# Kernel tuning notes

Hardware: AMD Instinct MI355X
Metric: run time of the kernel (lower is better)

The kernel has to match this reference:

```python
import jax, jax.numpy as jnp
import numpy as np

D_MODEL = 768
NUM_HEADS = 12
HEAD_DIM = D_MODEL // NUM_HEADS
B, S = 2, 2048


def setup_inputs() -> dict:
    key = jax.random.key(0)
    ks = jax.random.split(key, 12)
    s = 1.0 / np.sqrt(D_MODEL)
    inp = {
        "query": jax.random.normal(ks[0], (B, S, D_MODEL), jnp.float32),
        "key": jax.random.normal(ks[1], (B, S, D_MODEL), jnp.float32),
        "value": jax.random.normal(ks[2], (B, S, D_MODEL), jnp.float32),
        # causal mask; masked_fill(scores, mask == 0, -inf)
        "mask": jnp.tril(jnp.ones((S, S), jnp.int32))[None, None, :, :],
        "Wq": jax.random.uniform(ks[3], (D_MODEL, D_MODEL), jnp.float32, -s, s),
        "bq": jax.random.uniform(ks[4], (D_MODEL,), jnp.float32, -s, s),
        "Wk": jax.random.uniform(ks[5], (D_MODEL, D_MODEL), jnp.float32, -s, s),
        "bk": jax.random.uniform(ks[6], (D_MODEL,), jnp.float32, -s, s),
        "Wv": jax.random.uniform(ks[7], (D_MODEL, D_MODEL), jnp.float32, -s, s),
        "bv": jax.random.uniform(ks[8], (D_MODEL,), jnp.float32, -s, s),
        "Wo": jax.random.uniform(ks[9], (D_MODEL, D_MODEL), jnp.float32, -s, s),
        "bo": jax.random.uniform(ks[10], (D_MODEL,), jnp.float32, -s, s),
    }
    return inp


def reference(query, key, value, mask, Wq, bq, Wk, bk, Wv, bv, Wo, bo):
    Bq, Lq, Dm = query.shape
    Lk = key.shape[1]
    H, Dh = NUM_HEADS, HEAD_DIM
    # projections (torch Linear: x @ W.T + b), split into heads -> [B,H,L,Dh]
    q = (query @ Wq.T + bq).reshape(Bq, Lq, H, Dh).transpose(0, 2, 1, 3)
    k = (key @ Wk.T + bk).reshape(Bq, Lk, H, Dh).transpose(0, 2, 1, 3)
    v = (value @ Wv.T + bv).reshape(Bq, Lk, H, Dh).transpose(0, 2, 1, 3)
    scores = jnp.einsum("bhqd,bhkd->bhqk", q, k) / jnp.sqrt(jnp.float32(Dh))
    scores = jnp.where(mask == 0, -jnp.inf, scores)
    attn = jax.nn.softmax(scores, axis=-1)
    context = jnp.einsum("bhqk,bhkd->bhqd", attn, v)
    context = context.transpose(0, 2, 1, 3).reshape(Bq, Lq, Dm)
    return context @ Wo.T + bo
```

## Files before the change

### kernel.cpp

```cpp
#include <hip/hip_runtime.h>

#define DM    768
#define NH    12
#define NB    2
#define DHD   64
#define SQL   2048
#define MROWS 4096
#define WSZ   589824
#define XSZ   3145728
#define QSCALE 0.18033688f

typedef short  s16x8 __attribute__((ext_vector_type(8)));
typedef float  f32x4 __attribute__((ext_vector_type(4)));
typedef float  f32x16 __attribute__((ext_vector_type(16)));
typedef unsigned short u16x4 __attribute__((ext_vector_type(4)));
typedef unsigned short u16x8 __attribute__((ext_vector_type(8)));
typedef unsigned int   u32x4 __attribute__((ext_vector_type(4)));

static __device__ __forceinline__ unsigned short f2bf(float f) {
    unsigned int u = __builtin_bit_cast(unsigned int, f);
    u += 0x7FFFu + ((u >> 16) & 1u);
    return (unsigned short)(u >> 16);
}

static __device__ __forceinline__ unsigned int cvtpk1(float x, float y) {
    unsigned int r;
    asm("v_cvt_pk_bf16_f32 %0, %1, %2" : "=v"(r) : "v"(x), "v"(y));
    return r;
}

static __device__ __forceinline__ uint2 cvt2(float4 v) {
    return (uint2){cvtpk1(v.x, v.y), cvtpk1(v.z, v.w)};
}

static __device__ __forceinline__ f32x4 mfma16(s16x8 a, s16x8 b, f32x4 c) {
    return __builtin_amdgcn_mfma_f32_16x16x32_bf16(a, b, c, 0, 0, 0);
}
static __device__ __forceinline__ f32x16 mfma32(s16x8 a, s16x8 b, f32x16 c) {
    return __builtin_amdgcn_mfma_f32_32x32x16_bf16(a, b, c, 0, 0, 0);
}

__global__ __launch_bounds__(256)
void w_to_bf16(const float* __restrict__ Wq, const float* __restrict__ Wk,
               const float* __restrict__ Wv, const float* __restrict__ Wo,
               unsigned short* __restrict__ dst)
{
    const int z = blockIdx.y;
    const float* src = (z == 0) ? Wq : (z == 1) ? Wk : (z == 2) ? Wv : Wo;
    unsigned short* d = dst + (size_t)z * WSZ;
    const int nv = WSZ / 8;
    for (int i = blockIdx.x * 256 + threadIdx.x; i < nv; i += gridDim.x * 256) {
        float4 a = *reinterpret_cast<const float4*>(&src[(size_t)i * 8]);
        float4 b = *reinterpret_cast<const float4*>(&src[(size_t)i * 8 + 4]);
        uint2 p0 = cvt2(a), p1 = cvt2(b);
        u32x4 pk = {p0.x, p0.y, p1.x, p1.y};
        *reinterpret_cast<u32x4*>(&d[(size_t)i * 8]) = pk;
    }
}

__global__ __launch_bounds__(256)
void qkv_proj(const float* __restrict__ Xq, const float* __restrict__ Xk,
              const float* __restrict__ Xv,
              const unsigned short* __restrict__ Wb,
              const float* __restrict__ bq, const float* __restrict__ bk,
              const float* __restrict__ bv,
              unsigned short* __restrict__ Qo, unsigned short* __restrict__ Ko,
              unsigned short* __restrict__ Vo)
{
    const int z = blockIdx.z;
    const float* X = (z == 0) ? Xq : (z == 1) ? Xk : Xv;
    const unsigned short* W = Wb + (size_t)z * WSZ;
    const float* bias = (z == 0) ? bq : (z == 1) ? bk : bv;
    unsigned short* O = (z == 0) ? Qo : (z == 1) ? Ko : Vo;

    __shared__ unsigned short As[64][40];
    __shared__ unsigned short Bs[128][40];

    const int tid  = threadIdx.x;
    const int lane = tid & 63;
    const int w    = tid >> 6;
    const int wm   = w >> 1, wn = w & 1;
    const int l15  = lane & 15, lg = lane >> 4;
    const int m0   = blockIdx.y * 64;
    const int n0   = blockIdx.x * 128;
    const int arr  = tid >> 3, arc = (tid & 7) << 2;
    const int brr  = tid >> 2, brc = (tid & 3) << 3;

    f32x4 acc[2][4];
    #pragma unroll
    for (int i = 0; i < 2; ++i)
        #pragma unroll
        for (int j = 0; j < 4; ++j)
            acc[i][j] = (f32x4){0.f, 0.f, 0.f, 0.f};

    float4 ra[2]; u16x8 rb[2];
    #pragma unroll
    for (int i = 0; i < 2; ++i) {
        ra[i] = *reinterpret_cast<const float4*>(&X[(size_t)(m0 + arr + i * 32) * DM + arc]);
        rb[i] = *reinterpret_cast<const u16x8*>(&W[(size_t)(n0 + brr + i * 64) * DM + brc]);
    }
    #pragma unroll
    for (int i = 0; i < 2; ++i) {
        *reinterpret_cast<uint2*>(&As[arr + i * 32][arc]) = cvt2(ra[i]);
        *reinterpret_cast<u16x8*>(&Bs[brr + i * 64][brc]) = rb[i];
    }
    __syncthreads();

    for (int k0 = 0; k0 < DM; k0 += 32) {
        const bool more = (k0 + 32 < DM);
        if (more) {
            #pragma unroll
            for (int i = 0; i < 2; ++i) {
                ra[i] = *reinterpret_cast<const float4*>(&X[(size_t)(m0 + arr + i * 32) * DM + k0 + 32 + arc]);
                rb[i] = *reinterpret_cast<const u16x8*>(&W[(size_t)(n0 + brr + i * 64) * DM + k0 + 32 + brc]);
            }
        }
        s16x8 af[2], bfg[4];
        #pragma unroll
        for (int mi = 0; mi < 2; ++mi)
            af[mi] = *reinterpret_cast<const s16x8*>(&As[wm * 32 + mi * 16 + l15][lg * 8]);
        #pragma unroll
        for (int nj = 0; nj < 4; ++nj)
            bfg[nj] = *reinterpret_cast<const s16x8*>(&Bs[wn * 64 + nj * 16 + l15][lg * 8]);
        #pragma unroll
        for (int mi = 0; mi < 2; ++mi)
            #pragma unroll
            for (int nj = 0; nj < 4; ++nj)
                acc[mi][nj] = mfma16(af[mi], bfg[nj], acc[mi][nj]);
        __syncthreads();
        if (more) {
            #pragma unroll
            for (int i = 0; i < 2; ++i) {
                *reinterpret_cast<uint2*>(&As[arr + i * 32][arc]) = cvt2(ra[i]);
                *reinterpret_cast<u16x8*>(&Bs[brr + i * 64][brc]) = rb[i];
            }
            __syncthreads();
        }
    }

    const float scale = (z == 0) ? QSCALE : 1.0f;
    #pragma unroll
    for (int mi = 0; mi < 2; ++mi) {
        #pragma unroll
        for (int nj = 0; nj < 4; ++nj) {
            int col = n0 + wn * 64 + nj * 16 + l15;
            float bb = bias[col];
            int hh = col >> 6, d = col & 63;
            #pragma unroll
            for (int r = 0; r < 4; ++r) {
                int row = m0 + wm * 32 + mi * 16 + (lg << 2) + r;
                float v = (acc[mi][nj][r] + bb) * scale;
                unsigned short hv = f2bf(v);
                int b = row >> 11, s = row & (SQL - 1);
                if (z < 2)
                    O[(((size_t)(b * NH + hh) * SQL) + s) * DHD + d] = hv;
                else
                    O[(((size_t)(b * NH + hh) * DHD) + d) * SQL + s] = hv;
            }
        }
    }
}

__global__ __launch_bounds__(256)
void attn(const unsigned short* __restrict__ Q, const unsigned short* __restrict__ K,
          const unsigned short* __restrict__ Vt, unsigned short* __restrict__ Ctx)
{
    __shared__ float Acc[4][2112];

    const int tid  = threadIdx.x;
    const int lane = tid & 63;
    const int w    = tid >> 6;
    const int hi   = lane >> 5;
    const int l31  = lane & 31;
    const int q0   = (gridDim.x - 1 - blockIdx.x) * 32;
    const int bh   = blockIdx.y;

    const unsigned short* Qb = Q  + (size_t)bh * SQL * DHD;
    const unsigned short* Kb = K  + (size_t)bh * SQL * DHD;
    const unsigned short* Vb = Vt + (size_t)bh * DHD * SQL;

    s16x8 qf[4];
    #pragma unroll
    for (int t = 0; t < 4; ++t)
        qf[t] = *reinterpret_cast<const s16x8*>(&Qb[(size_t)(q0 + l31) * DHD + t * 16 + hi * 8]);

    f32x16 o0 = {}, o1 = {};
    float m = -__builtin_inff(), l = 0.f;
    const int nkt = (q0 >> 5) + 1;

    s16x8 kf[4], knx[4];
    if (w < nkt) {
        const int kv0 = w * 32;
        #pragma unroll
        for (int t = 0; t < 4; ++t)
            kf[t] = *reinterpret_cast<const s16x8*>(&Kb[(size_t)(kv0 + l31) * DHD + t * 16 + hi * 8]);
    }

    for (int kt = w; kt < nkt; kt += 4) {
        const int kv0 = kt * 32;

        f32x16 s = {};
        #pragma unroll
        for (int t = 0; t < 4; ++t)
            s = mfma32(kf[t], qf[t], s);

        const int ktn = kt + 4;
        if (ktn < nkt) {
            const int kvn = ktn * 32;
            #pragma unroll
            for (int t = 0; t < 4; ++t)
                knx[t] = *reinterpret_cast<const s16x8*>(&Kb[(size_t)(kvn + l31) * DHD + t * 16 + hi * 8]);
        }

        s16x8 vf00 = *reinterpret_cast<const s16x8*>(&Vb[(size_t)(l31)      * SQL + kv0 + hi * 8]);
        s16x8 vf01 = *reinterpret_cast<const s16x8*>(&Vb[(size_t)(l31)      * SQL + kv0 + 16 + hi * 8]);
        s16x8 vf10 = *reinterpret_cast<const s16x8*>(&Vb[(size_t)(32 + l31) * SQL + kv0 + hi * 8]);
        s16x8 vf11 = *reinterpret_cast<const s16x8*>(&Vb[(size_t)(32 + l31) * SQL + kv0 + 16 + hi * 8]);

        if (kt == nkt - 1) {
            #pragma unroll
            for (int r = 0; r < 16; ++r) {
                int kvr = (r & 3) + 8 * (r >> 2) + 4 * hi;
                if (kvr > l31) s[r] = -1.0e30f;
            }
        }

        float pm = s[0];
        #pragma unroll
        for (int r = 1; r < 16; ++r) pm = fmaxf(pm, s[r]);
        pm = fmaxf(pm, __shfl_xor(pm, 32));
        const float mn = fmaxf(m, pm);
        const float al = __builtin_amdgcn_exp2f(m - mn);
        m = mn;

        float rs = 0.f;
        #pragma unroll
        for (int r = 0; r < 16; ++r) {
            s[r] = __builtin_amdgcn_exp2f(s[r] - mn);
            rs += s[r];
        }
        rs += __shfl_xor(rs, 32);
        l = l * al + rs;

        #pragma unroll
        for (int r = 0; r < 16; ++r) { o0[r] *= al; o1[r] *= al; }

        s16x8 pf[2];
        #pragma unroll
        for (int ks = 0; ks < 2; ++ks) {
            const int rb = ks * 8;
            unsigned int a0 = cvtpk1(s[rb + 0], s[rb + 1]);
            unsigned int b0 = cvtpk1(s[rb + 4], s[rb + 5]);
            asm("v_permlane32_swap_b32 %0, %1" : "+v"(a0), "+v"(b0));
            unsigned int a1 = cvtpk1(s[rb + 2], s[rb + 3]);
            unsigned int b1 = cvtpk1(s[rb + 6], s[rb + 7]);
            asm("v_permlane32_swap_b32 %0, %1" : "+v"(a1), "+v"(b1));
            u32x4 pw = {a0, a1, b0, b1};
            pf[ks] = __builtin_bit_cast(s16x8, pw);
        }

        o0 = mfma32(vf00, pf[0], o0);
        o0 = mfma32(vf01, pf[1], o0);
        o1 = mfma32(vf10, pf[0], o1);
        o1 = mfma32(vf11, pf[1], o1);

        if (ktn < nkt) {
            #pragma unroll
            for (int t = 0; t < 4; ++t) kf[t] = knx[t];
        }
    }

    #pragma unroll
    for (int r = 0; r < 16; ++r) {
        int d = (r & 3) + 8 * (r >> 2) + 4 * hi;
        Acc[w][d * 32 + l31]        = o0[r];
        Acc[w][(32 + d) * 32 + l31] = o1[r];
    }
    if (hi == 0) { Acc[w][2048 + l31] = m; Acc[w][2080 + l31] = l; }
    __syncthreads();

    {
        const int q  = tid & 31;
        const int d8 = tid >> 5;
        float mv[4], lv[4];
        #pragma unroll
        for (int j = 0; j < 4; ++j) {
            mv[j] = Acc[j][2048 + q];
            lv[j] = Acc[j][2080 + q];
        }
        float M = fmaxf(fmaxf(mv[0], mv[1]), fmaxf(mv[2], mv[3]));
        float f[4]; float L = 0.f;
        #pragma unroll
        for (int j = 0; j < 4; ++j) {
            f[j] = __builtin_amdgcn_exp2f(mv[j] - M);
            L += f[j] * lv[j];
        }
        const float invL = 1.0f / L;
        const int b = bh / NH, h = bh % NH;
        u16x8 pk;
        #pragma unroll
        for (int jj = 0; jj < 8; ++jj) {
            int d = d8 * 8 + jj;
            float o = 0.f;
            #pragma unroll
            for (int j = 0; j < 4; ++j) o += f[j] * Acc[j][d * 32 + q];
            pk[jj] = f2bf(o * invL);
        }
        *reinterpret_cast<u16x8*>(&Ctx[(((size_t)(b * SQL + q0 + q) * NH) + h) * DHD + d8 * 8]) = pk;
    }
}

__global__ __launch_bounds__(256)
void out_proj(const unsigned short* __restrict__ Ctx, const unsigned short* __restrict__ Wob,
              const float* __restrict__ bo, float* __restrict__ Out)
{
    __shared__ unsigned short As[64][40];
    __shared__ unsigned short Bs[128][40];

    const int tid  = threadIdx.x;
    const int lane = tid & 63;
    const int w    = tid >> 6;
    const int wm   = w >> 1, wn = w & 1;
    const int l15  = lane & 15, lg = lane >> 4;
    const int m0   = blockIdx.y * 64;
    const int n0   = blockIdx.x * 128;
    const int arr  = tid >> 2, arc = (tid & 3) << 3;
    const int brr  = tid >> 2, brc = (tid & 3) << 3;

    f32x4 acc[2][4];
    #pragma unroll
    for (int i = 0; i < 2; ++i)
        #pragma unroll
        for (int j = 0; j < 4; ++j)
            acc[i][j] = (f32x4){0.f, 0.f, 0.f, 0.f};

    u16x8 ra; u16x8 rb[2];
    ra = *reinterpret_cast<const u16x8*>(&Ctx[(size_t)(m0 + arr) * DM + arc]);
    #pragma unroll
    for (int i = 0; i < 2; ++i)
        rb[i] = *reinterpret_cast<const u16x8*>(&Wob[(size_t)(n0 + brr + i * 64) * DM + brc]);
    *reinterpret_cast<u16x8*>(&As[arr][arc]) = ra;
    #pragma unroll
    for (int i = 0; i < 2; ++i)
        *reinterpret_cast<u16x8*>(&Bs[brr + i * 64][brc]) = rb[i];
    __syncthreads();

    for (int k0 = 0; k0 < DM; k0 += 32) {
        const bool more = (k0 + 32 < DM);
        if (more) {
            ra = *reinterpret_cast<const u16x8*>(&Ctx[(size_t)(m0 + arr) * DM + k0 + 32 + arc]);
            #pragma unroll
            for (int i = 0; i < 2; ++i)
                rb[i] = *reinterpret_cast<const u16x8*>(&Wob[(size_t)(n0 + brr + i * 64) * DM + k0 + 32 + brc]);
        }
        s16x8 af[2], bfg[4];
        #pragma unroll
        for (int mi = 0; mi < 2; ++mi)
            af[mi] = *reinterpret_cast<const s16x8*>(&As[wm * 32 + mi * 16 + l15][lg * 8]);
        #pragma unroll
        for (int nj = 0; nj < 4; ++nj)
            bfg[nj] = *reinterpret_cast<const s16x8*>(&Bs[wn * 64 + nj * 16 + l15][lg * 8]);
        #pragma unroll
        for (int mi = 0; mi < 2; ++mi)
            #pragma unroll
            for (int nj = 0; nj < 4; ++nj)
                acc[mi][nj] = mfma16(af[mi], bfg[nj], acc[mi][nj]);
        __syncthreads();
        if (more) {
            *reinterpret_cast<u16x8*>(&As[arr][arc]) = ra;
            #pragma unroll
            for (int i = 0; i < 2; ++i)
                *reinterpret_cast<u16x8*>(&Bs[brr + i * 64][brc]) = rb[i];
            __syncthreads();
        }
    }

    #pragma unroll
    for (int mi = 0; mi < 2; ++mi)
        #pragma unroll
        for (int nj = 0; nj < 4; ++nj) {
            int col = n0 + wn * 64 + nj * 16 + l15;
            float bb = bo[col];
            #pragma unroll
            for (int r = 0; r < 4; ++r) {
                int row = m0 + wm * 32 + mi * 16 + (lg << 2) + r;
                Out[(size_t)row * DM + col] = acc[mi][nj][r] + bb;
            }
        }
}

extern "C" void kernel_launch(void* const* d_in, const int* in_sizes, int n_in,
                              void* d_out, int out_size, void* d_ws, size_t ws_size,
                              hipStream_t stream) {
    const float* query = (const float*)d_in[0];
    const float* key   = (const float*)d_in[1];
    const float* value = (const float*)d_in[2];
    const float* Wq = (const float*)d_in[4];
    const float* bq = (const float*)d_in[5];
    const float* Wk = (const float*)d_in[6];
    const float* bk = (const float*)d_in[7];
    const float* Wv = (const float*)d_in[8];
    const float* bv = (const float*)d_in[9];
    const float* Wo = (const float*)d_in[10];
    const float* bo = (const float*)d_in[11];
    float* out = (float*)d_out;

    unsigned short* Wb  = (unsigned short*)d_ws;
    unsigned short* Qb  = Wb  + (size_t)4 * WSZ;
    unsigned short* Kb  = Qb  + (size_t)XSZ;
    unsigned short* Vtb = Kb  + (size_t)XSZ;
    unsigned short* Ctx = Vtb + (size_t)XSZ;

    w_to_bf16<<<dim3(72, 4), 256, 0, stream>>>(Wq, Wk, Wv, Wo, Wb);
    qkv_proj<<<dim3(6, 64, 3), 256, 0, stream>>>(query, key, value, Wb,
                                                 bq, bk, bv, Qb, Kb, Vtb);
    attn<<<dim3(64, NB * NH), 256, 0, stream>>>(Qb, Kb, Vtb, Ctx);
    out_proj<<<dim3(6, 64), 256, 0, stream>>>(Ctx, Wb + (size_t)3 * WSZ, bo, out);
}
```

Measured before the change: 264.6 us.

## Pre-convert inputs to bf16, widen GEMM K-tiles, double attention waves

```diff
diff --git a/kernel.cpp b/kernel.cpp
--- a/kernel.cpp
+++ b/kernel.cpp
@@ -41,26 +41,37 @@
 }
 
 __global__ __launch_bounds__(256)
-void w_to_bf16(const float* __restrict__ Wq, const float* __restrict__ Wk,
-               const float* __restrict__ Wv, const float* __restrict__ Wo,
-               unsigned short* __restrict__ dst)
+void prep(const float* __restrict__ Xq, const float* __restrict__ Xk,
+          const float* __restrict__ Xv,
+          const float* __restrict__ Wq, const float* __restrict__ Wk,
+          const float* __restrict__ Wv, const float* __restrict__ Wo,
+          unsigned short* __restrict__ Xb, unsigned short* __restrict__ Wb)
 {
-    const int z = blockIdx.y;
-    const float* src = (z == 0) ? Wq : (z == 1) ? Wk : (z == 2) ? Wv : Wo;
-    unsigned short* d = dst + (size_t)z * WSZ;
-    const int nv = WSZ / 8;
+    const int y = blockIdx.y;
+    const float* src;
+    unsigned short* dst;
+    int nv;
+    if (y < 3) {
+        src = (y == 0) ? Xq : (y == 1) ? Xk : Xv;
+        dst = Xb + (size_t)y * XSZ;
+        nv = XSZ / 8;
+    } else {
+        const int z = y - 3;
+        src = (z == 0) ? Wq : (z == 1) ? Wk : (z == 2) ? Wv : Wo;
+        dst = Wb + (size_t)z * WSZ;
+        nv = WSZ / 8;
+    }
     for (int i = blockIdx.x * 256 + threadIdx.x; i < nv; i += gridDim.x * 256) {
         float4 a = *reinterpret_cast<const float4*>(&src[(size_t)i * 8]);
         float4 b = *reinterpret_cast<const float4*>(&src[(size_t)i * 8 + 4]);
         uint2 p0 = cvt2(a), p1 = cvt2(b);
         u32x4 pk = {p0.x, p0.y, p1.x, p1.y};
-        *reinterpret_cast<u32x4*>(&d[(size_t)i * 8]) = pk;
+        *reinterpret_cast<u32x4*>(&dst[(size_t)i * 8]) = pk;
     }
 }
 
 __global__ __launch_bounds__(256)
-void qkv_proj(const float* __restrict__ Xq, const float* __restrict__ Xk,
-              const float* __restrict__ Xv,
+void qkv_proj(const unsigned short* __restrict__ Xb,
               const unsigned short* __restrict__ Wb,
               const float* __restrict__ bq, const float* __restrict__ bk,
               const float* __restrict__ bv,
@@ -68,13 +79,13 @@
               unsigned short* __restrict__ Vo)
 {
     const int z = blockIdx.z;
-    const float* X = (z == 0) ? Xq : (z == 1) ? Xk : Xv;
+    const unsigned short* X = Xb + (size_t)z * XSZ;
     const unsigned short* W = Wb + (size_t)z * WSZ;
     const float* bias = (z == 0) ? bq : (z == 1) ? bk : bv;
     unsigned short* O = (z == 0) ? Qo : (z == 1) ? Ko : Vo;
 
-    __shared__ unsigned short As[64][40];
-    __shared__ unsigned short Bs[128][40];
+    __shared__ unsigned short As[64][72];
+    __shared__ unsigned short Bs[128][72];
 
     const int tid  = threadIdx.x;
     const int lane = tid & 63;
@@ -83,8 +94,8 @@
     const int l15  = lane & 15, lg = lane >> 4;
     const int m0   = blockIdx.y * 64;
     const int n0   = blockIdx.x * 128;
-    const int arr  = tid >> 3, arc = (tid & 7) << 2;
-    const int brr  = tid >> 2, brc = (tid & 3) << 3;
+    const int ar   = tid >> 2, ac = (tid & 3) << 4;
+    const int br   = tid >> 1, bc = (tid & 1) << 5;
 
     f32x4 acc[2][4];
     #pragma unroll
@@ -93,47 +104,57 @@
         for (int j = 0; j < 4; ++j)
             acc[i][j] = (f32x4){0.f, 0.f, 0.f, 0.f};
 
-    float4 ra[2]; u16x8 rb[2];
-    #pragma unroll
-    for (int i = 0; i < 2; ++i) {
-        ra[i] = *reinterpret_cast<const float4*>(&X[(size_t)(m0 + arr + i * 32) * DM + arc]);
-        rb[i] = *reinterpret_cast<const u16x8*>(&W[(size_t)(n0 + brr + i * 64) * DM + brc]);
-    }
-    #pragma unroll
-    for (int i = 0; i < 2; ++i) {
-        *reinterpret_cast<uint2*>(&As[arr + i * 32][arc]) = cvt2(ra[i]);
-        *reinterpret_cast<u16x8*>(&Bs[brr + i * 64][brc]) = rb[i];
-    }
+    u16x8 ra[2], rb[4];
+    #pragma unroll
+    for (int i = 0; i < 2; ++i)
+        ra[i] = *reinterpret_cast<const u16x8*>(&X[(size_t)(m0 + ar) * DM + ac + i * 8]);
+    #pragma unroll
+    for (int i = 0; i < 4; ++i)
+        rb[i] = *reinterpret_cast<const u16x8*>(&W[(size_t)(n0 + br) * DM + bc + i * 8]);
+    #pragma unroll
+    for (int i = 0; i < 2; ++i)
+        *reinterpret_cast<u16x8*>(&As[ar][ac + i * 8]) = ra[i];
+    #pragma unroll
+    for (int i = 0; i < 4; ++i)
+        *reinterpret_cast<u16x8*>(&Bs[br][bc + i * 8]) = rb[i];
     __syncthreads();
 
-    for (int k0 = 0; k0 < DM; k0 += 32) {
-        const bool more = (k0 + 32 < DM);
+    for (int k0 = 0; k0 < DM; k0 += 64) {
+        const bool more = (k0 + 64 < DM);
         if (more) {
             #pragma unroll
-            for (int i = 0; i < 2; ++i) {
-                ra[i] = *reinterpret_cast<const float4*>(&X[(size_t)(m0 + arr + i * 32) * DM + k0 + 32 + arc]);
-                rb[i] = *reinterpret_cast<const u16x8*>(&W[(size_t)(n0 + brr + i * 64) * DM + k0 + 32 + brc]);
-            }
-        }
-        s16x8 af[2], bfg[4];
+            for (int i = 0; i < 2; ++i)
+                ra[i] = *reinterpret_cast<const u16x8*>(&X[(size_t)(m0 + ar) * DM + k0 + 64 + ac + i * 8]);
+            #pragma unroll
+            for (int i = 0; i < 4; ++i)
+                rb[i] = *reinterpret_cast<const u16x8*>(&W[(size_t)(n0 + br) * DM + k0 + 64 + bc + i * 8]);
+        }
+        s16x8 af[2][2], bfg[4][2];
         #pragma unroll
         for (int mi = 0; mi < 2; ++mi)
-            af[mi] = *reinterpret_cast<const s16x8*>(&As[wm * 32 + mi * 16 + l15][lg * 8]);
+            #pragma unroll
+            for (int ks = 0; ks < 2; ++ks)
+                af[mi][ks] = *reinterpret_cast<const s16x8*>(&As[wm * 32 + mi * 16 + l15][ks * 32 + lg * 8]);
         #pragma unroll
         for (int nj = 0; nj < 4; ++nj)
-            bfg[nj] = *reinterpret_cast<const s16x8*>(&Bs[wn * 64 + nj * 16 + l15][lg * 8]);
+            #pragma unroll
+            for (int ks = 0; ks < 2; ++ks)
+                bfg[nj][ks] = *reinterpret_cast<const s16x8*>(&Bs[wn * 64 + nj * 16 + l15][ks * 32 + lg * 8]);
         #pragma unroll
         for (int mi = 0; mi < 2; ++mi)
             #pragma unroll
             for (int nj = 0; nj < 4; ++nj)
-                acc[mi][nj] = mfma16(af[mi], bfg[nj], acc[mi][nj]);
+                #pragma unroll
+                for (int ks = 0; ks < 2; ++ks)
+                    acc[mi][nj] = mfma16(af[mi][ks], bfg[nj][ks], acc[mi][nj]);
         __syncthreads();
         if (more) {
             #pragma unroll
-            for (int i = 0; i < 2; ++i) {
-                *reinterpret_cast<uint2*>(&As[arr + i * 32][arc]) = cvt2(ra[i]);
-                *reinterpret_cast<u16x8*>(&Bs[brr + i * 64][brc]) = rb[i];
-            }
+            for (int i = 0; i < 2; ++i)
+                *reinterpret_cast<u16x8*>(&As[ar][ac + i * 8]) = ra[i];
+            #pragma unroll
+            for (int i = 0; i < 4; ++i)
+                *reinterpret_cast<u16x8*>(&Bs[br][bc + i * 8]) = rb[i];
             __syncthreads();
         }
     }
@@ -146,26 +167,31 @@
             int col = n0 + wn * 64 + nj * 16 + l15;
             float bb = bias[col];
             int hh = col >> 6, d = col & 63;
-            #pragma unroll
-            for (int r = 0; r < 4; ++r) {
-                int row = m0 + wm * 32 + mi * 16 + (lg << 2) + r;
-                float v = (acc[mi][nj][r] + bb) * scale;
-                unsigned short hv = f2bf(v);
+            if (z < 2) {
+                #pragma unroll
+                for (int r = 0; r < 4; ++r) {
+                    int row = m0 + wm * 32 + mi * 16 + (lg << 2) + r;
+                    int b = row >> 11, s = row & (SQL - 1);
+                    O[(((size_t)(b * NH + hh) * SQL) + s) * DHD + d] =
+                        f2bf((acc[mi][nj][r] + bb) * scale);
+                }
+            } else {
+                int row = m0 + wm * 32 + mi * 16 + (lg << 2);
                 int b = row >> 11, s = row & (SQL - 1);
-                if (z < 2)
-                    O[(((size_t)(b * NH + hh) * SQL) + s) * DHD + d] = hv;
-                else
-                    O[(((size_t)(b * NH + hh) * DHD) + d) * SQL + s] = hv;
-            }
-        }
-    }
-}
-
-__global__ __launch_bounds__(256)
+                u16x4 pk;
+                #pragma unroll
+                for (int r = 0; r < 4; ++r) pk[r] = f2bf(acc[mi][nj][r] + bb);
+                *reinterpret_cast<u16x4*>(&O[(((size_t)(b * NH + hh) * DHD) + d) * SQL + s]) = pk;
+            }
+        }
+    }
+}
+
+__global__ __launch_bounds__(512)
 void attn(const unsigned short* __restrict__ Q, const unsigned short* __restrict__ K,
           const unsigned short* __restrict__ Vt, unsigned short* __restrict__ Ctx)
 {
-    __shared__ float Acc[4][2112];
+    __shared__ float Acc[8][2112];
 
     const int tid  = threadIdx.x;
     const int lane = tid & 63;
@@ -188,46 +214,44 @@
     float m = -__builtin_inff(), l = 0.f;
     const int nkt = (q0 >> 5) + 1;
 
-    s16x8 kf[4], knx[4];
-    if (w < nkt) {
-        const int kv0 = w * 32;
-        #pragma unroll
-        for (int t = 0; t < 4; ++t)
-            kf[t] = *reinterpret_cast<const s16x8*>(&Kb[(size_t)(kv0 + l31) * DHD + t * 16 + hi * 8]);
-    }
-
-    for (int kt = w; kt < nkt; kt += 4) {
-        const int kv0 = kt * 32;
-
-        f32x16 s = {};
-        #pragma unroll
-        for (int t = 0; t < 4; ++t)
-            s = mfma32(kf[t], qf[t], s);
-
-        const int ktn = kt + 4;
-        if (ktn < nkt) {
-            const int kvn = ktn * 32;
-            #pragma unroll
-            for (int t = 0; t < 4; ++t)
-                knx[t] = *reinterpret_cast<const s16x8*>(&Kb[(size_t)(kvn + l31) * DHD + t * 16 + hi * 8]);
-        }
-
-        s16x8 vf00 = *reinterpret_cast<const s16x8*>(&Vb[(size_t)(l31)      * SQL + kv0 + hi * 8]);
-        s16x8 vf01 = *reinterpret_cast<const s16x8*>(&Vb[(size_t)(l31)      * SQL + kv0 + 16 + hi * 8]);
-        s16x8 vf10 = *reinterpret_cast<const s16x8*>(&Vb[(size_t)(32 + l31) * SQL + kv0 + hi * 8]);
-        s16x8 vf11 = *reinterpret_cast<const s16x8*>(&Vb[(size_t)(32 + l31) * SQL + kv0 + 16 + hi * 8]);
-
-        if (kt == nkt - 1) {
+    int cnt = (w < nkt) ? ((nkt - w + 7) >> 3) : 0;
+    int kt  = w;
+
+    while (cnt >= 2) {
+        const int ka = kt * 32, kb2 = (kt + 8) * 32;
+
+        s16x8 kfa[4], kfb[4];
+        #pragma unroll
+        for (int t = 0; t < 4; ++t) {
+            kfa[t] = *reinterpret_cast<const s16x8*>(&Kb[(size_t)(ka + l31) * DHD + t * 16 + hi * 8]);
+            kfb[t] = *reinterpret_cast<const s16x8*>(&Kb[(size_t)(kb2 + l31) * DHD + t * 16 + hi * 8]);
+        }
+        s16x8 va00 = *reinterpret_cast<const s16x8*>(&Vb[(size_t)(l31)      * SQL + ka + hi * 8]);
+        s16x8 va01 = *reinterpret_cast<const s16x8*>(&Vb[(size_t)(l31)      * SQL + ka + 16 + hi * 8]);
+        s16x8 va10 = *reinterpret_cast<const s16x8*>(&Vb[(size_t)(32 + l31) * SQL + ka + hi * 8]);
+        s16x8 va11 = *reinterpret_cast<const s16x8*>(&Vb[(size_t)(32 + l31) * SQL + ka + 16 + hi * 8]);
+        s16x8 vb00 = *reinterpret_cast<const s16x8*>(&Vb[(size_t)(l31)      * SQL + kb2 + hi * 8]);
+        s16x8 vb01 = *reinterpret_cast<const s16x8*>(&Vb[(size_t)(l31)      * SQL + kb2 + 16 + hi * 8]);
+        s16x8 vb10 = *reinterpret_cast<const s16x8*>(&Vb[(size_t)(32 + l31) * SQL + kb2 + hi * 8]);
+        s16x8 vb11 = *reinterpret_cast<const s16x8*>(&Vb[(size_t)(32 + l31) * SQL + kb2 + 16 + hi * 8]);
+
+        f32x16 sa = {}, sb = {};
+        #pragma unroll
+        for (int t = 0; t < 4; ++t) sa = mfma32(kfa[t], qf[t], sa);
+        #pragma unroll
+        for (int t = 0; t < 4; ++t) sb = mfma32(kfb[t], qf[t], sb);
+
+        if (kt + 8 == nkt - 1) {
             #pragma unroll
             for (int r = 0; r < 16; ++r) {
                 int kvr = (r & 3) + 8 * (r >> 2) + 4 * hi;
-                if (kvr > l31) s[r] = -1.0e30f;
-            }
-        }
-
-        float pm = s[0];
-        #pragma unroll
-        for (int r = 1; r < 16; ++r) pm = fmaxf(pm, s[r]);
+                if (kvr > l31) sb[r] = -1.0e30f;
+            }
+        }
+
+        float pm = fmaxf(sa[0], sb[0]);
+        #pragma unroll
+        for (int r = 1; r < 16; ++r) pm = fmaxf(pm, fmaxf(sa[r], sb[r]));
         pm = fmaxf(pm, __shfl_xor(pm, 32));
         const float mn = fmaxf(m, pm);
         const float al = __builtin_amdgcn_exp2f(m - mn);
@@ -236,8 +260,8 @@
         float rs = 0.f;
         #pragma unroll
         for (int r = 0; r < 16; ++r) {
-            s[r] = __builtin_amdgcn_exp2f(s[r] - mn);
-            rs += s[r];
+            sa[r] = __builtin_amdgcn_exp2f(sa[r] - mn); rs += sa[r];
+            sb[r] = __builtin_amdgcn_exp2f(sb[r] - mn); rs += sb[r];
         }
         rs += __shfl_xor(rs, 32);
         l = l * al + rs;
@@ -245,29 +269,104 @@
         #pragma unroll
         for (int r = 0; r < 16; ++r) { o0[r] *= al; o1[r] *= al; }
 
-        s16x8 pf[2];
+        s16x8 pfa[2], pfb[2];
         #pragma unroll
         for (int ks = 0; ks < 2; ++ks) {
             const int rb = ks * 8;
-            unsigned int a0 = cvtpk1(s[rb + 0], s[rb + 1]);
-            unsigned int b0 = cvtpk1(s[rb + 4], s[rb + 5]);
+            unsigned int a0 = cvtpk1(sa[rb + 0], sa[rb + 1]);
+            unsigned int b0 = cvtpk1(sa[rb + 4], sa[rb + 5]);
             asm("v_permlane32_swap_b32 %0, %1" : "+v"(a0), "+v"(b0));
-            unsigned int a1 = cvtpk1(s[rb + 2], s[rb + 3]);
-            unsigned int b1 = cvtpk1(s[rb + 6], s[rb + 7]);
+            unsigned int a1 = cvtpk1(sa[rb + 2], sa[rb + 3]);
+            unsigned int b1 = cvtpk1(sa[rb + 6], sa[rb + 7]);
             asm("v_permlane32_swap_b32 %0, %1" : "+v"(a1), "+v"(b1));
             u32x4 pw = {a0, a1, b0, b1};
-            pf[ks] = __builtin_bit_cast(s16x8, pw);
-        }
-
-        o0 = mfma32(vf00, pf[0], o0);
-        o0 = mfma32(vf01, pf[1], o0);
-        o1 = mfma32(vf10, pf[0], o1);
-        o1 = mfma32(vf11, pf[1], o1);
-
-        if (ktn < nkt) {
-            #pragma unroll
-            for (int t = 0; t < 4; ++t) kf[t] = knx[t];
-        }
+            pfa[ks] = __builtin_bit_cast(s16x8, pw);
+        }
+        #pragma unroll
+        for (int ks = 0; ks < 2; ++ks) {
+            const int rb = ks * 8;
+            unsigned int a0 = cvtpk1(sb[rb + 0], sb[rb + 1]);
+            unsigned int b0 = cvtpk1(sb[rb + 4], sb[rb + 5]);
+            asm("v_permlane32_swap_b32 %0, %1" : "+v"(a0), "+v"(b0));
+            unsigned int a1 = cvtpk1(sb[rb + 2], sb[rb + 3]);
+            unsigned int b1 = cvtpk1(sb[rb + 6], sb[rb + 7]);
+            asm("v_permlane32_swap_b32 %0, %1" : "+v"(a1), "+v"(b1));
+            u32x4 pw = {a0, a1, b0, b1};
+            pfb[ks] = __builtin_bit_cast(s16x8, pw);
+        }
+
+        o0 = mfma32(va00, pfa[0], o0);
+        o0 = mfma32(va01, pfa[1], o0);
+        o1 = mfma32(va10, pfa[0], o1);
+        o1 = mfma32(va11, pfa[1], o1);
+        o0 = mfma32(vb00, pfb[0], o0);
+        o0 = mfma32(vb01, pfb[1], o0);
+        o1 = mfma32(vb10, pfb[0], o1);
+        o1 = mfma32(vb11, pfb[1], o1);
+
+        kt += 16; cnt -= 2;
+    }
+
+    if (cnt) {
+        const int ka = kt * 32;
+        s16x8 kfa[4];
+        #pragma unroll
+        for (int t = 0; t < 4; ++t)
+            kfa[t] = *reinterpret_cast<const s16x8*>(&Kb[(size_t)(ka + l31) * DHD + t * 16 + hi * 8]);
+        s16x8 va00 = *reinterpret_cast<const s16x8*>(&Vb[(size_t)(l31)      * SQL + ka + hi * 8]);
+        s16x8 va01 = *reinterpret_cast<const s16x8*>(&Vb[(size_t)(l31)      * SQL + ka + 16 + hi * 8]);
+        s16x8 va10 = *reinterpret_cast<const s16x8*>(&Vb[(size_t)(32 + l31) * SQL + ka + hi * 8]);
+        s16x8 va11 = *reinterpret_cast<const s16x8*>(&Vb[(size_t)(32 + l31) * SQL + ka + 16 + hi * 8]);
+
+        f32x16 sa = {};
+        #pragma unroll
+        for (int t = 0; t < 4; ++t) sa = mfma32(kfa[t], qf[t], sa);
+
+        if (kt == nkt - 1) {
+            #pragma unroll
+            for (int r = 0; r < 16; ++r) {
+                int kvr = (r & 3) + 8 * (r >> 2) + 4 * hi;
+                if (kvr > l31) sa[r] = -1.0e30f;
+            }
+        }
+
+        float pm = sa[0];
+        #pragma unroll
+        for (int r = 1; r < 16; ++r) pm = fmaxf(pm, sa[r]);
+        pm = fmaxf(pm, __shfl_xor(pm, 32));
+        const float mn = fmaxf(m, pm);
+        const float al = __builtin_amdgcn_exp2f(m - mn);
+        m = mn;
+
+        float rs = 0.f;
+        #pragma unroll
+        for (int r = 0; r < 16; ++r) {
+            sa[r] = __builtin_amdgcn_exp2f(sa[r] - mn); rs += sa[r];
+        }
+        rs += __shfl_xor(rs, 32);
+        l = l * al + rs;
+
+        #pragma unroll
+        for (int r = 0; r < 16; ++r) { o0[r] *= al; o1[r] *= al; }
+
+        s16x8 pfa[2];
+        #pragma unroll
+        for (int ks = 0; ks < 2; ++ks) {
+            const int rb = ks * 8;
+            unsigned int a0 = cvtpk1(sa[rb + 0], sa[rb + 1]);
+            unsigned int b0 = cvtpk1(sa[rb + 4], sa[rb + 5]);
+            asm("v_permlane32_swap_b32 %0, %1" : "+v"(a0), "+v"(b0));
+            unsigned int a1 = cvtpk1(sa[rb + 2], sa[rb + 3]);
+            unsigned int b1 = cvtpk1(sa[rb + 6], sa[rb + 7]);
+            asm("v_permlane32_swap_b32 %0, %1" : "+v"(a1), "+v"(b1));
+            u32x4 pw = {a0, a1, b0, b1};
+            pfa[ks] = __builtin_bit_cast(s16x8, pw);
+        }
+
+        o0 = mfma32(va00, pfa[0], o0);
+        o0 = mfma32(va01, pfa[1], o0);
+        o1 = mfma32(va10, pfa[0], o1);
+        o1 = mfma32(va11, pfa[1], o1);
     }
 
     #pragma unroll
@@ -281,32 +380,29 @@
 
     {
         const int q  = tid & 31;
-        const int d8 = tid >> 5;
-        float mv[4], lv[4];
-        #pragma unroll
-        for (int j = 0; j < 4; ++j) {
-            mv[j] = Acc[j][2048 + q];
-            lv[j] = Acc[j][2080 + q];
-        }
-        float M = fmaxf(fmaxf(mv[0], mv[1]), fmaxf(mv[2], mv[3]));
-        float f[4]; float L = 0.f;
-        #pragma unroll
-        for (int j = 0; j < 4; ++j) {
+        const int d4 = (tid >> 5) << 2;
+        float M = -__builtin_inff();
+        float mv[8];
+        #pragma unroll
+        for (int j = 0; j < 8; ++j) { mv[j] = Acc[j][2048 + q]; M = fmaxf(M, mv[j]); }
+        float f[8]; float L = 0.f;
+        #pragma unroll
+        for (int j = 0; j < 8; ++j) {
             f[j] = __builtin_amdgcn_exp2f(mv[j] - M);
-            L += f[j] * lv[j];
+            L += f[j] * Acc[j][2080 + q];
         }
         const float invL = 1.0f / L;
         const int b = bh / NH, h = bh % NH;
-        u16x8 pk;
-        #pragma unroll
-        for (int jj = 0; jj < 8; ++jj) {
-            int d = d8 * 8 + jj;
+        u16x4 pk;
+        #pragma unroll
+        for (int jj = 0; jj < 4; ++jj) {
+            int d = d4 + jj;
             float o = 0.f;
             #pragma unroll
-            for (int j = 0; j < 4; ++j) o += f[j] * Acc[j][d * 32 + q];
+            for (int j = 0; j < 8; ++j) o += f[j] * Acc[j][d * 32 + q];
             pk[jj] = f2bf(o * invL);
         }
-        *reinterpret_cast<u16x8*>(&Ctx[(((size_t)(b * SQL + q0 + q) * NH) + h) * DHD + d8 * 8]) = pk;
+        *reinterpret_cast<u16x4*>(&Ctx[(((size_t)(b * SQL + q0 + q) * NH) + h) * DHD + d4]) = pk;
     }
 }
 
@@ -314,8 +410,8 @@
 void out_proj(const unsigned short* __restrict__ Ctx, const unsigned short* __restrict__ Wob,
               const float* __restrict__ bo, float* __restrict__ Out)
 {
-    __shared__ unsigned short As[64][40];
-    __shared__ unsigned short Bs[128][40];
+    __shared__ unsigned short As[64][72];
+    __shared__ unsigned short Bs[64][72];
 
     const int tid  = threadIdx.x;
     const int lane = tid & 63;
@@ -323,54 +419,60 @@
     const int wm   = w >> 1, wn = w & 1;
     const int l15  = lane & 15, lg = lane >> 4;
     const int m0   = blockIdx.y * 64;
-    const int n0   = blockIdx.x * 128;
-    const int arr  = tid >> 2, arc = (tid & 3) << 3;
-    const int brr  = tid >> 2, brc = (tid & 3) << 3;
-
-    f32x4 acc[2][4];
+    const int n0   = blockIdx.x * 64;
+    const int ar   = tid >> 2, ac = (tid & 3) << 4;
+
+    f32x4 acc[2][2];
     #pragma unroll
     for (int i = 0; i < 2; ++i)
         #pragma unroll
-        for (int j = 0; j < 4; ++j)
+        for (int j = 0; j < 2; ++j)
             acc[i][j] = (f32x4){0.f, 0.f, 0.f, 0.f};
 
-    u16x8 ra; u16x8 rb[2];
-    ra = *reinterpret_cast<const u16x8*>(&Ctx[(size_t)(m0 + arr) * DM + arc]);
-    #pragma unroll
-    for (int i = 0; i < 2; ++i)
-        rb[i] = *reinterpret_cast<const u16x8*>(&Wob[(size_t)(n0 + brr + i * 64) * DM + brc]);
-    *reinterpret_cast<u16x8*>(&As[arr][arc]) = ra;
-    #pragma unroll
-    for (int i = 0; i < 2; ++i)
-        *reinterpret_cast<u16x8*>(&Bs[brr + i * 64][brc]) = rb[i];
+    u16x8 ra[2], rb[2];
+    #pragma unroll
+    for (int i = 0; i < 2; ++i) {
+        ra[i] = *reinterpret_cast<const u16x8*>(&Ctx[(size_t)(m0 + ar) * DM + ac + i * 8]);
+        rb[i] = *reinterpret_cast<const u16x8*>(&Wob[(size_t)(n0 + ar) * DM + ac + i * 8]);
+    }
+    #pragma unroll
+    for (int i = 0; i < 2; ++i) {
+        *reinterpret_cast<u16x8*>(&As[ar][ac + i * 8]) = ra[i];
+        *reinterpret_cast<u16x8*>(&Bs[ar][ac + i * 8]) = rb[i];
+    }
     __syncthreads();
 
-    for (int k0 = 0; k0 < DM; k0 += 32) {
-        const bool more = (k0 + 32 < DM);
+    for (int k0 = 0; k0 < DM; k0 += 64) {
+        const bool more = (k0 + 64 < DM);
         if (more) {
-            ra = *reinterpret_cast<const u16x8*>(&Ctx[(size_t)(m0 + arr) * DM + k0 + 32 + arc]);
-            #pragma unroll
-            for (int i = 0; i < 2; ++i)
-                rb[i] = *reinterpret_cast<const u16x8*>(&Wob[(size_t)(n0 + brr + i * 64) * DM + k0 + 32 + brc]);
-        }
-        s16x8 af[2], bfg[4];
+            #pragma unroll
+            for (int i = 0; i < 2; ++i) {
+                ra[i] = *reinterpret_cast<const u16x8*>(&Ctx[(size_t)(m0 + ar) * DM + k0 + 64 + ac + i * 8]);
+                rb[i] = *reinterpret_cast<const u16x8*>(&Wob[(size_t)(n0 + ar) * DM + k0 + 64 + ac + i * 8]);
+            }
+        }
+        s16x8 af[2][2], bfg[2][2];
         #pragma unroll
         for (int mi = 0; mi < 2; ++mi)
-            af[mi] = *reinterpret_cast<const s16x8*>(&As[wm * 32 + mi * 16 + l15][lg * 8]);
-        #pragma unroll
-        for (int nj = 0; nj < 4; ++nj)
-            bfg[nj] = *reinterpret_cast<const s16x8*>(&Bs[wn * 64 + nj * 16 + l15][lg * 8]);
+            #pragma unroll
+            for (int ks = 0; ks < 2; ++ks) {
+                af[mi][ks]  = *reinterpret_cast<const s16x8*>(&As[wm * 32 + mi * 16 + l15][ks * 32 + lg * 8]);
+                bfg[mi][ks] = *reinterpret_cast<const s16x8*>(&Bs[wn * 32 + mi * 16 + l15][ks * 32 + lg * 8]);
+            }
         #pragma unroll
         for (int mi = 0; mi < 2; ++mi)
             #pragma unroll
-            for (int nj = 0; nj < 4; ++nj)
-                acc[mi][nj] = mfma16(af[mi], bfg[nj], acc[mi][nj]);
+            for (int nj = 0; nj < 2; ++nj)
+                #pragma unroll
+                for (int ks = 0; ks < 2; ++ks)
+                    acc[mi][nj] = mfma16(af[mi][ks], bfg[nj][ks], acc[mi][nj]);
         __syncthreads();
         if (more) {
-            *reinterpret_cast<u16x8*>(&As[arr][arc]) = ra;
-            #pragma unroll
-            for (int i = 0; i < 2; ++i)
-                *reinterpret_cast<u16x8*>(&Bs[brr + i * 64][brc]) = rb[i];
+            #pragma unroll
+            for (int i = 0; i < 2; ++i) {
+                *reinterpret_cast<u16x8*>(&As[ar][ac + i * 8]) = ra[i];
+                *reinterpret_cast<u16x8*>(&Bs[ar][ac + i * 8]) = rb[i];
+            }
             __syncthreads();
         }
     }
@@ -378,8 +480,8 @@
     #pragma unroll
     for (int mi = 0; mi < 2; ++mi)
         #pragma unroll
-        for (int nj = 0; nj < 4; ++nj) {
-            int col = n0 + wn * 64 + nj * 16 + l15;
+        for (int nj = 0; nj < 2; ++nj) {
+            int col = n0 + wn * 32 + nj * 16 + l15;
             float bb = bo[col];
             #pragma unroll
             for (int r = 0; r < 4; ++r) {
@@ -406,14 +508,14 @@
     float* out = (float*)d_out;
 
     unsigned short* Wb  = (unsigned short*)d_ws;
-    unsigned short* Qb  = Wb  + (size_t)4 * WSZ;
+    unsigned short* Xb  = Wb  + (size_t)4 * WSZ;
+    unsigned short* Qb  = Xb  + (size_t)3 * XSZ;
     unsigned short* Kb  = Qb  + (size_t)XSZ;
     unsigned short* Vtb = Kb  + (size_t)XSZ;
-    unsigned short* Ctx = Vtb + (size_t)XSZ;
-
-    w_to_bf16<<<dim3(72, 4), 256, 0, stream>>>(Wq, Wk, Wv, Wo, Wb);
-    qkv_proj<<<dim3(6, 64, 3), 256, 0, stream>>>(query, key, value, Wb,
-                                                 bq, bk, bv, Qb, Kb, Vtb);
-    attn<<<dim3(64, NB * NH), 256, 0, stream>>>(Qb, Kb, Vtb, Ctx);
-    out_proj<<<dim3(6, 64), 256, 0, stream>>>(Ctx, Wb + (size_t)3 * WSZ, bo, out);
-}
+    unsigned short* Ctx = Xb;
+
+    prep<<<dim3(384, 7), 256, 0, stream>>>(query, key, value, Wq, Wk, Wv, Wo, Xb, Wb);
+    qkv_proj<<<dim3(6, 64, 3), 256, 0, stream>>>(Xb, Wb, bq, bk, bv, Qb, Kb, Vtb);
+    attn<<<dim3(64, NB * NH), 512, 0, stream>>>(Qb, Kb, Vtb, Ctx);
+    out_proj<<<dim3(12, 64), 256, 0, stream>>>(Ctx, Wb + (size_t)3 * WSZ, bo, out);
+}
```

Result: faster. 248.9 us (-5.9%).
